# Kernel optimization log

Hardware: AMD Instinct MI355X
Metric: run time of the kernel (lower is better)

The kernel has to match this reference:

```python
import jax, jax.numpy as jnp
import numpy as np

D_MODEL = 1024
N_HEADS = 16
HEAD_DIM = D_MODEL // N_HEADS
BATCH = 1
SEQLEN = 4096


def setup_inputs() -> dict:
    key = jax.random.key(0)
    k1, k2, k3 = jax.random.split(key, 3)
    x = jax.random.normal(k1, (BATCH, SEQLEN, D_MODEL), dtype=jnp.float32)
    # match typical Dense init scale so softmax isn't saturated
    Wqkv = jax.random.normal(k2, (D_MODEL, 3 * D_MODEL), dtype=jnp.float32) / np.sqrt(D_MODEL)
    Wout = jax.random.normal(k3, (D_MODEL, D_MODEL), dtype=jnp.float32) / np.sqrt(D_MODEL)
    return {"x": x, "Wqkv": Wqkv, "Wout": Wout}


def reference(x, Wqkv, Wout):
    b, l, d = x.shape
    qkv = x @ Wqkv  # [b, l, 3d]
    q, k, v = jnp.split(qkv, 3, axis=-1)
    # [b, l, d] -> [b, h, l, hd]
    def to_heads(t):
        return t.reshape(b, l, N_HEADS, HEAD_DIM).transpose(0, 2, 1, 3)
    q, k, v = to_heads(q), to_heads(k), to_heads(v)
    scale = 1.0 / np.sqrt(HEAD_DIM)
    attn = jnp.einsum('bhld,bhsd->bhls', q, k) * scale  # [b,h,l,l]
    causal_mask = jnp.tril(jnp.ones((l, l), dtype=bool))
    attn = jnp.where(causal_mask, attn, -jnp.inf)
    attn = jax.nn.softmax(attn, axis=-1)
    out = jnp.einsum('bhls,bhsd->bhld', attn, v)  # [b,h,l,hd]
    out = out.transpose(0, 2, 1, 3).reshape(b, l, d)
    return out @ Wout
```

## Files before the change

kernel.cpp:

```cpp
#include <hip/hip_runtime.h>

#define SEQ 4096
#define DM 1024
#define NH 16
#define HD 64

typedef __attribute__((ext_vector_type(8))) short short8;
typedef __attribute__((ext_vector_type(4))) short short4v;
typedef __attribute__((ext_vector_type(2))) short short2v;
typedef __attribute__((ext_vector_type(4))) float float4v;
typedef __attribute__((ext_vector_type(4))) int int4v;

__device__ __forceinline__ short f2bf(float f) {
    union { float f; unsigned u; } v; v.f = f;
    unsigned u = v.u;
    return (short)((u + 0x7fffu + ((u >> 16) & 1u)) >> 16);
}
__device__ __forceinline__ int cvtpk(float lo, float hi) {
    int r;
    asm("v_cvt_pk_bf16_f32 %0, %1, %2" : "=v"(r) : "v"(lo), "v"(hi));
    return r;
}

__device__ __forceinline__ void gload_lds16(const void* g, void* l) {
    __builtin_amdgcn_global_load_lds(
        (const __attribute__((address_space(1))) void*)g,
        (__attribute__((address_space(3))) void*)l, 16, 0, 0);
}

__global__ void cast_x(const float* __restrict__ in, short* __restrict__ out, int n4) {
    int i = blockIdx.x * blockDim.x + threadIdx.x;
    if (i < n4) {
        float4v x = ((const float4v*)in)[i];
        short4v o;
        o[0] = f2bf(x[0]); o[1] = f2bf(x[1]); o[2] = f2bf(x[2]); o[3] = f2bf(x[3]);
        ((short4v*)out)[i] = o;
    }
}

__global__ void transpose_cast(const float* __restrict__ in, short* __restrict__ out,
                               int H, int W, int scaled_rows, float scale) {
    __shared__ float tile[32][33];
    int bx = blockIdx.x * 32, by = blockIdx.y * 32;
    int tx = threadIdx.x, ty = threadIdx.y;
#pragma unroll
    for (int i = 0; i < 32; i += 8)
        tile[ty + i][tx] = in[(by + ty + i) * W + bx + tx];
    __syncthreads();
#pragma unroll
    for (int i = 0; i < 32; i += 8) {
        int orow = bx + ty + i;
        float sc = (orow < scaled_rows) ? scale : 1.0f;
        out[orow * H + by + tx] = f2bf(tile[tx][ty + i] * sc);
    }
}

__global__ void transpose_v(const short* __restrict__ qkv, short* __restrict__ vt) {
    __shared__ short tile[64][66];
    int h = blockIdx.z;
    int l0 = blockIdx.x * 64;
    int tx = threadIdx.x, ty = threadIdx.y;
#pragma unroll
    for (int i = 0; i < 8; i++) {
        int r = ty + i * 8;
        short2v v = *(const short2v*)&qkv[(l0 + r) * (3 * DM) + 2 * DM + h * HD + 2 * tx];
        tile[r][2 * tx] = v[0];
        tile[r][2 * tx + 1] = v[1];
    }
    __syncthreads();
#pragma unroll
    for (int i = 0; i < 8; i++) {
        int d = ty + i * 8;
        short2v v;
        v[0] = tile[2 * tx][d];
        v[1] = tile[2 * tx + 1][d];
        int s = l0 + 2 * tx;
        int soff = (s & ~31) | ((s & 12) << 1) | ((s & 16) >> 2) | (s & 3);
        *(short2v*)&vt[(h * HD + d) * SEQ + soff] = v;
    }
}

template <typename OutT>
__global__ __launch_bounds__(256) void gemm_bt(const short* __restrict__ A,
                                               const short* __restrict__ BT,
                                               OutT* __restrict__ C,
                                               int M, int N, int K) {
    __shared__ short As[128 * 64];
    __shared__ short Bs[128 * 64];
    int tid  = threadIdx.x;
    int m0   = blockIdx.y * 128;
    int n0   = blockIdx.x * 128;
    int w    = tid >> 6, lane = tid & 63;
    int wm   = w >> 1,  wn   = w & 1;
    int quad = lane >> 4, l15 = lane & 15;
    int lrow = lane >> 3;
    int cg   = (lane & 7) ^ lrow;
    int xr   = (l15 & 7) * 8;

    float4v acc[4][4];
#pragma unroll
    for (int mi = 0; mi < 4; mi++)
#pragma unroll
        for (int ni = 0; ni < 4; ni++)
            acc[mi][ni] = {0.f, 0.f, 0.f, 0.f};

    for (int k0 = 0; k0 < K; k0 += 64) {
        __syncthreads();
#pragma unroll
        for (int t = 0; t < 4; t++) {
            int c = w * 4 + t;
            int r = c * 8 + lrow;
            gload_lds16(&A[(m0 + r) * K + k0 + cg * 8], &As[c * 8 * 64]);
            gload_lds16(&BT[(n0 + r) * K + k0 + cg * 8], &Bs[c * 8 * 64]);
        }
        __syncthreads();
        short8 a[4][2], b[4][2];
#pragma unroll
        for (int mi = 0; mi < 4; mi++)
#pragma unroll
            for (int kk = 0; kk < 2; kk++)
                a[mi][kk] = *(const short8*)&As[(wm * 64 + mi * 16 + l15) * 64 + (((kk * 4 + quad) * 8) ^ xr)];
#pragma unroll
        for (int ni = 0; ni < 4; ni++)
#pragma unroll
            for (int kk = 0; kk < 2; kk++)
                b[ni][kk] = *(const short8*)&Bs[(wn * 64 + ni * 16 + l15) * 64 + (((kk * 4 + quad) * 8) ^ xr)];
#pragma unroll
        for (int kk = 0; kk < 2; kk++)
#pragma unroll
            for (int mi = 0; mi < 4; mi++)
#pragma unroll
                for (int ni = 0; ni < 4; ni++)
                    acc[mi][ni] = __builtin_amdgcn_mfma_f32_16x16x32_bf16(a[mi][kk], b[ni][kk], acc[mi][ni], 0, 0, 0);
    }

#pragma unroll
    for (int mi = 0; mi < 4; mi++)
#pragma unroll
        for (int ni = 0; ni < 4; ni++)
#pragma unroll
            for (int r = 0; r < 4; r++) {
                int row = m0 + wm * 64 + mi * 16 + quad * 4 + r;
                int col = n0 + wn * 64 + ni * 16 + l15;
                float v = acc[mi][ni][r];
                if constexpr (sizeof(OutT) == 2) C[row * N + col] = (OutT)f2bf(v);
                else                             C[row * N + col] = (OutT)v;
            }
}

__global__ __launch_bounds__(256) void gemm_bt64(const short* __restrict__ A,
                                                 const short* __restrict__ BT,
                                                 float* __restrict__ C,
                                                 int M, int N, int K) {
    __shared__ short As[64 * 64];
    __shared__ short Bs[128 * 64];
    int tid  = threadIdx.x;
    int m0   = blockIdx.y * 64;
    int n0   = blockIdx.x * 128;
    int w    = tid >> 6, lane = tid & 63;
    int wm   = w >> 1,  wn   = w & 1;
    int quad = lane >> 4, l15 = lane & 15;
    int lrow = lane >> 3;
    int cg   = (lane & 7) ^ lrow;
    int xr   = (l15 & 7) * 8;

    float4v acc[2][4];
#pragma unroll
    for (int mi = 0; mi < 2; mi++)
#pragma unroll
        for (int ni = 0; ni < 4; ni++)
            acc[mi][ni] = {0.f, 0.f, 0.f, 0.f};

    for (int k0 = 0; k0 < K; k0 += 64) {
        __syncthreads();
#pragma unroll
        for (int t = 0; t < 2; t++) {
            int c = w * 2 + t;
            int r = c * 8 + lrow;
            gload_lds16(&A[(m0 + r) * K + k0 + cg * 8], &As[c * 8 * 64]);
        }
#pragma unroll
        for (int t = 0; t < 4; t++) {
            int c = w * 4 + t;
            int r = c * 8 + lrow;
            gload_lds16(&BT[(n0 + r) * K + k0 + cg * 8], &Bs[c * 8 * 64]);
        }
        __syncthreads();
        short8 a[2][2], b[4][2];
#pragma unroll
        for (int mi = 0; mi < 2; mi++)
#pragma unroll
            for (int kk = 0; kk < 2; kk++)
                a[mi][kk] = *(const short8*)&As[(wm * 32 + mi * 16 + l15) * 64 + (((kk * 4 + quad) * 8) ^ xr)];
#pragma unroll
        for (int ni = 0; ni < 4; ni++)
#pragma unroll
            for (int kk = 0; kk < 2; kk++)
                b[ni][kk] = *(const short8*)&Bs[(wn * 64 + ni * 16 + l15) * 64 + (((kk * 4 + quad) * 8) ^ xr)];
#pragma unroll
        for (int kk = 0; kk < 2; kk++)
#pragma unroll
            for (int mi = 0; mi < 2; mi++)
#pragma unroll
                for (int ni = 0; ni < 4; ni++)
                    acc[mi][ni] = __builtin_amdgcn_mfma_f32_16x16x32_bf16(a[mi][kk], b[ni][kk], acc[mi][ni], 0, 0, 0);
    }

#pragma unroll
    for (int mi = 0; mi < 2; mi++)
#pragma unroll
        for (int ni = 0; ni < 4; ni++)
#pragma unroll
            for (int r = 0; r < 4; r++) {
                int row = m0 + wm * 32 + mi * 16 + quad * 4 + r;
                int col = n0 + wn * 64 + ni * 16 + l15;
                C[row * N + col] = acc[mi][ni][r];
            }
}

__global__ __launch_bounds__(256, 2) void attn_kernel(const short* __restrict__ qkv,
                                                      const short* __restrict__ vtp,
                                                      float* __restrict__ Of0,
                                                      float* __restrict__ Of1,
                                                      float* __restrict__ Of2,
                                                      float* __restrict__ Lf0,
                                                      float* __restrict__ Lf1,
                                                      float* __restrict__ Lf2) {
    __shared__ short Ks[3][64 * 64];
    __shared__ short Vs[3][64 * 64];
    int gid = blockIdx.x;
    int rr = gid & 7, qq = gid >> 3;
    int hb = qq / 48;
    int rem = qq - hb * 48;
    int h = rr + 8 * hb;
    int b = rem & 15;
    int j = rem >> 4;
    float* __restrict__ Of = (j == 0) ? Of0 : (j == 1) ? Of1 : Of2;
    float* __restrict__ Lf = (j == 0) ? Lf0 : (j == 1) ? Lf1 : Lf2;
    int B0 = 2 * b + 2;

    int tid = threadIdx.x;
    int w = tid >> 6, lane = tid & 63;
    int quad = lane >> 4, l15 = lane & 15;
    int rowb = w * 16;
    int lrow = lane >> 3;
    int cg   = (lane & 7) ^ lrow;
    int xr   = (l15 & 7) * 8;

    const short* Kg = qkv + DM + h * HD;
    const short* Vg = vtp + (h * HD) * SEQ;

    short8 onesv;
#pragma unroll
    for (int i = 0; i < 8; i++) onesv[i] = (short)0x3F80;

#pragma unroll 1
    for (int sg = 0; sg < 2; sg++) {
        int t, st0, stN;
        if (sg == 0) {
            t = b;
            st0 = 22 * j;
            stN = (22 * j + 22 < B0) ? 22 * j + 22 : B0;
        } else {
            t = 31 - b;
            int a0 = 22 * j - B0;
            st0 = (a0 > 0) ? a0 : 0;
            stN = 22 * j + 22 - B0;
        }
        if (st0 >= stN) continue;

        int q0 = t * 128;
        int qw = q0 + w * 32;

        short8 aq[2][2];
#pragma unroll
        for (int mi = 0; mi < 2; mi++)
#pragma unroll
            for (int kk = 0; kk < 2; kk++)
                aq[mi][kk] = *(const short8*)&qkv[(qw + mi * 16 + l15) * (3 * DM) + h * HD + kk * 32 + quad * 8];

        float4v lacc[2];
        float4v o[2][4];
#pragma unroll
        for (int mi = 0; mi < 2; mi++) {
            lacc[mi] = {0.f, 0.f, 0.f, 0.f};
#pragma unroll
            for (int dt = 0; dt < 4; dt++)
                o[mi][dt] = {0.f, 0.f, 0.f, 0.f};
        }

        auto stage = [&](int slot, int tt_) {
            int s0_ = tt_ * 64;
#pragma unroll
            for (int i = 0; i < 2; i++) {
                int r = rowb + i * 8;
                gload_lds16(&Kg[(s0_ + r + lrow) * (3 * DM) + cg * 8], &Ks[slot][r * 64]);
                gload_lds16(&Vg[(r + lrow) * SEQ + s0_ + cg * 8],      &Vs[slot][r * 64]);
            }
        };

        stage(0, st0);
        bool two = (st0 + 1 < stN);
        if (two) {
            stage(1, st0 + 1);
            asm volatile("s_waitcnt vmcnt(4)" ::: "memory");
        } else {
            asm volatile("s_waitcnt vmcnt(0)" ::: "memory");
        }
        __builtin_amdgcn_s_barrier();
        __builtin_amdgcn_sched_barrier(0);

        short8 pa_p[2][2];
        short8 vc_p[8];
        int si = 0;
        for (int tt = st0; tt < stN; tt++) {
            int s0 = tt * 64;
            int s2 = si + 2; if (s2 >= 3) s2 -= 3;
            bool haveStage = (tt + 2 < stN);
            if (haveStage) stage(s2, tt + 2);

            const short* Kb = &Ks[si][0];
            const short* Vb = &Vs[si][0];

            short8 kc[8];
#pragma unroll
            for (int ni = 0; ni < 4; ni++)
#pragma unroll
                for (int kk = 0; kk < 2; kk++)
                    kc[ni * 2 + kk] = *(const short8*)&Kb[(ni * 16 + l15) * 64 + (((kk * 4 + quad) * 8) ^ xr)];

            if (tt > st0) {
                __builtin_amdgcn_s_setprio(1);
#pragma unroll
                for (int mi = 0; mi < 2; mi++)
#pragma unroll
                    for (int pr = 0; pr < 2; pr++)
                        lacc[mi] = __builtin_amdgcn_mfma_f32_16x16x32_bf16(pa_p[mi][pr], onesv, lacc[mi], 0, 0, 0);
#pragma unroll
                for (int mi = 0; mi < 2; mi++)
#pragma unroll
                    for (int dt = 0; dt < 4; dt++)
#pragma unroll
                        for (int pr = 0; pr < 2; pr++)
                            o[mi][dt] = __builtin_amdgcn_mfma_f32_16x16x32_bf16(pa_p[mi][pr], vc_p[dt * 2 + pr], o[mi][dt], 0, 0, 0);
                __builtin_amdgcn_s_setprio(0);
            }

#pragma unroll
            for (int dt = 0; dt < 4; dt++)
#pragma unroll
                for (int pr = 0; pr < 2; pr++)
                    vc_p[dt * 2 + pr] = *(const short8*)&Vb[(dt * 16 + l15) * 64 + (((pr * 4 + quad) * 8) ^ xr)];

            float4v s[2][4];
            __builtin_amdgcn_s_setprio(1);
#pragma unroll
            for (int mi = 0; mi < 2; mi++)
#pragma unroll
                for (int ni = 0; ni < 4; ni++) {
                    float4v a = {0.f, 0.f, 0.f, 0.f};
#pragma unroll
                    for (int kk = 0; kk < 2; kk++)
                        a = __builtin_amdgcn_mfma_f32_16x16x32_bf16(kc[ni * 2 + kk], aq[mi][kk], a, 0, 0, 0);
                    s[mi][ni] = a;
                }
            __builtin_amdgcn_s_setprio(0);

            bool diag = (s0 + 63 > qw);
            if (diag) {
#pragma unroll
                for (int mi = 0; mi < 2; mi++) {
                    int qrow = qw + mi * 16 + l15;
#pragma unroll
                    for (int ni = 0; ni < 4; ni++)
#pragma unroll
                        for (int r = 0; r < 4; r++) {
                            float p = __builtin_amdgcn_exp2f(s[mi][ni][r]);
                            int scol = s0 + ni * 16 + quad * 4 + r;
                            s[mi][ni][r] = (scol <= qrow) ? p : 0.f;
                        }
                }
            } else {
#pragma unroll
                for (int mi = 0; mi < 2; mi++)
#pragma unroll
                    for (int ni = 0; ni < 4; ni++)
#pragma unroll
                        for (int r = 0; r < 4; r++)
                            s[mi][ni][r] = __builtin_amdgcn_exp2f(s[mi][ni][r]);
            }
#pragma unroll
            for (int mi = 0; mi < 2; mi++)
#pragma unroll
                for (int pr = 0; pr < 2; pr++) {
                    int4v wpk;
                    wpk[0] = cvtpk(s[mi][2 * pr][0], s[mi][2 * pr][1]);
                    wpk[1] = cvtpk(s[mi][2 * pr][2], s[mi][2 * pr][3]);
                    wpk[2] = cvtpk(s[mi][2 * pr + 1][0], s[mi][2 * pr + 1][1]);
                    wpk[3] = cvtpk(s[mi][2 * pr + 1][2], s[mi][2 * pr + 1][3]);
                    pa_p[mi][pr] = *(short8*)&wpk;
                }

            asm volatile("s_waitcnt lgkmcnt(0)" ::: "memory");
            if (haveStage) asm volatile("s_waitcnt vmcnt(4)" ::: "memory");
            else           asm volatile("s_waitcnt vmcnt(0)" ::: "memory");
            __builtin_amdgcn_s_barrier();
            __builtin_amdgcn_sched_barrier(0);
            si = si + 1; if (si >= 3) si = 0;
        }

        __builtin_amdgcn_s_setprio(1);
#pragma unroll
        for (int mi = 0; mi < 2; mi++)
#pragma unroll
            for (int pr = 0; pr < 2; pr++)
                lacc[mi] = __builtin_amdgcn_mfma_f32_16x16x32_bf16(pa_p[mi][pr], onesv, lacc[mi], 0, 0, 0);
#pragma unroll
        for (int mi = 0; mi < 2; mi++)
#pragma unroll
            for (int dt = 0; dt < 4; dt++)
#pragma unroll
                for (int pr = 0; pr < 2; pr++)
                    o[mi][dt] = __builtin_amdgcn_mfma_f32_16x16x32_bf16(pa_p[mi][pr], vc_p[dt * 2 + pr], o[mi][dt], 0, 0, 0);
        __builtin_amdgcn_s_setprio(0);

#pragma unroll
        for (int mi = 0; mi < 2; mi++)
#pragma unroll
            for (int r = 0; r < 4; r++) {
                int row = qw + mi * 16 + quad * 4 + r;
#pragma unroll
                for (int dt = 0; dt < 4; dt++)
                    Of[row * DM + h * HD + dt * 16 + l15] = o[mi][dt][r];
            }
        if (l15 == 0) {
#pragma unroll
            for (int mi = 0; mi < 2; mi++)
#pragma unroll
                for (int r = 0; r < 4; r++)
                    Lf[h * SEQ + qw + mi * 16 + quad * 4 + r] = lacc[mi][r];
        }
    }
}

__global__ void attn_finalize(const float* __restrict__ Of0, const float* __restrict__ Of1,
                              const float* __restrict__ Of2,
                              const float* __restrict__ Lf0, const float* __restrict__ Lf1,
                              const float* __restrict__ Lf2,
                              short* __restrict__ ao) {
    int i = blockIdx.x * blockDim.x + threadIdx.x;
    int q  = i >> 8;
    int c4 = i & 255;
    int h  = c4 >> 4;
    int t  = q >> 7;
    bool lowq = (t < 16);
    int b = lowq ? t : 31 - t;
    bool use0 = lowq || (b <= 9);
    bool use1 = (!lowq) || (b >= 11);
    bool use2 = !lowq;

    float l = 0.f;
    float4v acc = {0.f, 0.f, 0.f, 0.f};
    if (use0) {
        l += Lf0[h * SEQ + q];
        float4v a = ((const float4v*)Of0)[i];
        acc[0] += a[0]; acc[1] += a[1]; acc[2] += a[2]; acc[3] += a[3];
    }
    if (use1) {
        l += Lf1[h * SEQ + q];
        float4v a = ((const float4v*)Of1)[i];
        acc[0] += a[0]; acc[1] += a[1]; acc[2] += a[2]; acc[3] += a[3];
    }
    if (use2) {
        l += Lf2[h * SEQ + q];
        float4v a = ((const float4v*)Of2)[i];
        acc[0] += a[0]; acc[1] += a[1]; acc[2] += a[2]; acc[3] += a[3];
    }
    float inv = 1.0f / l;
    short4v o;
    o[0] = f2bf(acc[0] * inv);
    o[1] = f2bf(acc[1] * inv);
    o[2] = f2bf(acc[2] * inv);
    o[3] = f2bf(acc[3] * inv);
    ((short4v*)ao)[i] = o;
}

extern "C" void kernel_launch(void* const* d_in, const int* in_sizes, int n_in,
                              void* d_out, int out_size, void* d_ws, size_t ws_size,
                              hipStream_t stream) {
    const float* x    = (const float*)d_in[0];
    const float* Wqkv = (const float*)d_in[1];
    const float* Wout = (const float*)d_in[2];
    float* out = (float*)d_out;

    char* ws = (char*)d_ws;
    short* xb    = (short*)(ws);
    short* wqkvT = (short*)(ws + 8388608);
    float* Of0   = (float*)(ws);
    float* Of1   = (float*)(d_out);
    short* qkv   = (short*)(ws + 16777216);
    short* vt    = (short*)(ws + 41943040);
    short* ao    = (short*)(ws + 50331648);
    float* Of2   = (float*)(ws + 58720256);
    float* Lf0   = (float*)(ws + 75497472);
    float* Lf1   = (float*)(ws + 75759616);
    float* Lf2   = (float*)(ws + 76021760);
    short* woutT = (short*)(ws + 76283904);

    const float SC = 0.18033688011112042f;

    cast_x<<<4096, 256, 0, stream>>>(x, xb, (SEQ * DM) / 4);
    transpose_cast<<<dim3(3 * DM / 32, DM / 32), dim3(32, 8), 0, stream>>>(Wqkv, wqkvT, DM, 3 * DM, DM, SC);
    transpose_cast<<<dim3(DM / 32, DM / 32), dim3(32, 8), 0, stream>>>(Wout, woutT, DM, DM, 0, 1.0f);

    gemm_bt<short><<<dim3(3 * DM / 128, SEQ / 128), 256, 0, stream>>>(xb, wqkvT, qkv, SEQ, 3 * DM, DM);

    transpose_v<<<dim3(SEQ / 64, 1, NH), dim3(32, 8), 0, stream>>>(qkv, vt);

    attn_kernel<<<768, 256, 0, stream>>>(qkv, vt, Of0, Of1, Of2, Lf0, Lf1, Lf2);
    attn_finalize<<<(SEQ * DM / 4) / 256, 256, 0, stream>>>(Of0, Of1, Of2, Lf0, Lf1, Lf2, ao);

    gemm_bt64<<<dim3(DM / 128, SEQ / 64), 256, 0, stream>>>(ao, woutT, out, SEQ, DM, DM);
}
```

Measured before the change: 194.2 us.

## Fuse prep casts into one kernel and retile QKV GEMM to double-buffered 256x256

The x cast and the two weight transpose-casts are merged into one `prep` launch that dispatches on block index. The QKV projection GEMM moves from 128x128 tiles with 256 threads to 256x256 tiles with 512 threads. It now double-buffers its LDS stages so global-to-LDS loads for the next K slice overlap the MFMA work on the current one. This aims to cut launch overhead and raise data reuse per tile. The trade-off is that the grid shrinks to 192 blocks, fewer than the CU count, and each block uses about 128KB of LDS, which can leave CUs idle.

New measurement: 199.1 us. 1.03x slower.

```diff
diff --git a/kernel.cpp b/kernel.cpp
--- a/kernel.cpp
+++ b/kernel.cpp
@@ -28,21 +28,43 @@
         (__attribute__((address_space(3))) void*)l, 16, 0, 0);
 }
 
-__global__ void cast_x(const float* __restrict__ in, short* __restrict__ out, int n4) {
-    int i = blockIdx.x * blockDim.x + threadIdx.x;
-    if (i < n4) {
-        float4v x = ((const float4v*)in)[i];
+__global__ __launch_bounds__(256) void prep(const float* __restrict__ x,
+                                            const float* __restrict__ Wqkv,
+                                            const float* __restrict__ Wout,
+                                            short* __restrict__ xb,
+                                            short* __restrict__ wqkvT,
+                                            short* __restrict__ woutT) {
+    __shared__ float tile[32][33];
+    int bid = blockIdx.x;
+    int tid = threadIdx.x;
+    if (bid < 4096) {
+        int i = bid * 256 + tid;
+        float4v v = ((const float4v*)x)[i];
         short4v o;
-        o[0] = f2bf(x[0]); o[1] = f2bf(x[1]); o[2] = f2bf(x[2]); o[3] = f2bf(x[3]);
-        ((short4v*)out)[i] = o;
-    }
-}
-
-__global__ void transpose_cast(const float* __restrict__ in, short* __restrict__ out,
-                               int H, int W, int scaled_rows, float scale) {
-    __shared__ float tile[32][33];
-    int bx = blockIdx.x * 32, by = blockIdx.y * 32;
-    int tx = threadIdx.x, ty = threadIdx.y;
+        o[0] = f2bf(v[0]); o[1] = f2bf(v[1]); o[2] = f2bf(v[2]); o[3] = f2bf(v[3]);
+        ((short4v*)xb)[i] = o;
+        return;
+    }
+    const float* in;
+    short* out;
+    int W, bxi, byi;
+    float scale;
+    int scaled_rows;
+    if (bid < 4096 + 3072) {
+        int b = bid - 4096;
+        in = Wqkv; out = wqkvT; W = 3 * DM;
+        bxi = b % 96; byi = b / 96;
+        scale = 0.18033688011112042f;
+        scaled_rows = DM;
+    } else {
+        int b = bid - 7168;
+        in = Wout; out = woutT; W = DM;
+        bxi = b % 32; byi = b / 32;
+        scale = 1.0f;
+        scaled_rows = 0;
+    }
+    int bx = bxi * 32, by = byi * 32;
+    int tx = tid & 31, ty = tid >> 5;
 #pragma unroll
     for (int i = 0; i < 32; i += 8)
         tile[ty + i][tx] = in[(by + ty + i) * W + bx + tx];
@@ -51,7 +73,7 @@
     for (int i = 0; i < 32; i += 8) {
         int orow = bx + ty + i;
         float sc = (orow < scaled_rows) ? scale : 1.0f;
-        out[orow * H + by + tx] = f2bf(tile[tx][ty + i] * sc);
+        out[orow * DM + by + tx] = f2bf(tile[tx][ty + i] * sc);
     }
 }
 
@@ -80,71 +102,87 @@
     }
 }
 
-template <typename OutT>
-__global__ __launch_bounds__(256) void gemm_bt(const short* __restrict__ A,
-                                               const short* __restrict__ BT,
-                                               OutT* __restrict__ C,
-                                               int M, int N, int K) {
-    __shared__ short As[128 * 64];
-    __shared__ short Bs[128 * 64];
+__global__ __launch_bounds__(512, 2) void gemm_bt256(const short* __restrict__ A,
+                                                     const short* __restrict__ BT,
+                                                     short* __restrict__ C,
+                                                     int M, int N, int K) {
+    __shared__ short As[2][256 * 64];
+    __shared__ short Bs[2][256 * 64];
     int tid  = threadIdx.x;
-    int m0   = blockIdx.y * 128;
-    int n0   = blockIdx.x * 128;
+    int m0   = blockIdx.y * 256;
+    int n0   = blockIdx.x * 256;
     int w    = tid >> 6, lane = tid & 63;
-    int wm   = w >> 1,  wn   = w & 1;
+    int wm   = w >> 2,  wn   = w & 3;
     int quad = lane >> 4, l15 = lane & 15;
     int lrow = lane >> 3;
     int cg   = (lane & 7) ^ lrow;
     int xr   = (l15 & 7) * 8;
 
-    float4v acc[4][4];
-#pragma unroll
-    for (int mi = 0; mi < 4; mi++)
+    float4v acc[8][4];
+#pragma unroll
+    for (int mi = 0; mi < 8; mi++)
 #pragma unroll
         for (int ni = 0; ni < 4; ni++)
             acc[mi][ni] = {0.f, 0.f, 0.f, 0.f};
 
-    for (int k0 = 0; k0 < K; k0 += 64) {
-        __syncthreads();
+    auto stage = [&](int buf, int k0) {
 #pragma unroll
         for (int t = 0; t < 4; t++) {
             int c = w * 4 + t;
             int r = c * 8 + lrow;
-            gload_lds16(&A[(m0 + r) * K + k0 + cg * 8], &As[c * 8 * 64]);
-            gload_lds16(&BT[(n0 + r) * K + k0 + cg * 8], &Bs[c * 8 * 64]);
-        }
-        __syncthreads();
-        short8 a[4][2], b[4][2];
-#pragma unroll
-        for (int mi = 0; mi < 4; mi++)
+            gload_lds16(&A[(m0 + r) * K + k0 + cg * 8], &As[buf][c * 8 * 64]);
+            gload_lds16(&BT[(n0 + r) * K + k0 + cg * 8], &Bs[buf][c * 8 * 64]);
+        }
+    };
+
+    stage(0, 0);
+    asm volatile("s_waitcnt vmcnt(0)" ::: "memory");
+    __builtin_amdgcn_s_barrier();
+
+    int nk = K >> 6;
+    for (int kt = 0; kt < nk; kt++) {
+        int cur = kt & 1;
+        if (kt + 1 < nk) stage(cur ^ 1, (kt + 1) * 64);
+
+        const short* Ab = &As[cur][0];
+        const short* Bb = &Bs[cur][0];
+        short8 b[4][2];
+#pragma unroll
+        for (int ni = 0; ni < 4; ni++)
 #pragma unroll
             for (int kk = 0; kk < 2; kk++)
-                a[mi][kk] = *(const short8*)&As[(wm * 64 + mi * 16 + l15) * 64 + (((kk * 4 + quad) * 8) ^ xr)];
+                b[ni][kk] = *(const short8*)&Bb[(wn * 64 + ni * 16 + l15) * 64 + (((kk * 4 + quad) * 8) ^ xr)];
+#pragma unroll
+        for (int mh = 0; mh < 2; mh++) {
+            short8 a[4][2];
+#pragma unroll
+            for (int mi = 0; mi < 4; mi++)
+#pragma unroll
+                for (int kk = 0; kk < 2; kk++)
+                    a[mi][kk] = *(const short8*)&Ab[(wm * 128 + mh * 64 + mi * 16 + l15) * 64 + (((kk * 4 + quad) * 8) ^ xr)];
+#pragma unroll
+            for (int kk = 0; kk < 2; kk++)
+#pragma unroll
+                for (int mi = 0; mi < 4; mi++)
+#pragma unroll
+                    for (int ni = 0; ni < 4; ni++)
+                        acc[mh * 4 + mi][ni] = __builtin_amdgcn_mfma_f32_16x16x32_bf16(a[mi][kk], b[ni][kk], acc[mh * 4 + mi][ni], 0, 0, 0);
+        }
+
+        asm volatile("s_waitcnt lgkmcnt(0)" ::: "memory");
+        asm volatile("s_waitcnt vmcnt(0)" ::: "memory");
+        __builtin_amdgcn_s_barrier();
+    }
+
+#pragma unroll
+    for (int m8 = 0; m8 < 8; m8++)
 #pragma unroll
         for (int ni = 0; ni < 4; ni++)
 #pragma unroll
-            for (int kk = 0; kk < 2; kk++)
-                b[ni][kk] = *(const short8*)&Bs[(wn * 64 + ni * 16 + l15) * 64 + (((kk * 4 + quad) * 8) ^ xr)];
-#pragma unroll
-        for (int kk = 0; kk < 2; kk++)
-#pragma unroll
-            for (int mi = 0; mi < 4; mi++)
-#pragma unroll
-                for (int ni = 0; ni < 4; ni++)
-                    acc[mi][ni] = __builtin_amdgcn_mfma_f32_16x16x32_bf16(a[mi][kk], b[ni][kk], acc[mi][ni], 0, 0, 0);
-    }
-
-#pragma unroll
-    for (int mi = 0; mi < 4; mi++)
-#pragma unroll
-        for (int ni = 0; ni < 4; ni++)
-#pragma unroll
             for (int r = 0; r < 4; r++) {
-                int row = m0 + wm * 64 + mi * 16 + quad * 4 + r;
+                int row = m0 + wm * 128 + (m8 >> 2) * 64 + (m8 & 3) * 16 + quad * 4 + r;
                 int col = n0 + wn * 64 + ni * 16 + l15;
-                float v = acc[mi][ni][r];
-                if constexpr (sizeof(OutT) == 2) C[row * N + col] = (OutT)f2bf(v);
-                else                             C[row * N + col] = (OutT)v;
+                C[row * N + col] = f2bf(acc[m8][ni][r]);
             }
 }
 
@@ -507,13 +545,9 @@
     float* Lf2   = (float*)(ws + 76021760);
     short* woutT = (short*)(ws + 76283904);
 
-    const float SC = 0.18033688011112042f;
-
-    cast_x<<<4096, 256, 0, stream>>>(x, xb, (SEQ * DM) / 4);
-    transpose_cast<<<dim3(3 * DM / 32, DM / 32), dim3(32, 8), 0, stream>>>(Wqkv, wqkvT, DM, 3 * DM, DM, SC);
-    transpose_cast<<<dim3(DM / 32, DM / 32), dim3(32, 8), 0, stream>>>(Wout, woutT, DM, DM, 0, 1.0f);
-
-    gemm_bt<short><<<dim3(3 * DM / 128, SEQ / 128), 256, 0, stream>>>(xb, wqkvT, qkv, SEQ, 3 * DM, DM);
+    prep<<<8192, 256, 0, stream>>>(x, Wqkv, Wout, xb, wqkvT, woutT);
+
+    gemm_bt256<<<dim3(3 * DM / 256, SEQ / 256), 512, 0, stream>>>(xb, wqkvT, qkv, SEQ, 3 * DM, DM);
 
     transpose_v<<<dim3(SEQ / 64, 1, NH), dim3(32, 8), 0, stream>>>(qkv, vt);
 
```
